# Performance work log

Measured on AMD Instinct MI355X. Metric: run time of the kernel, lower is better.

Reference implementation:

```python
import jax, jax.numpy as jnp
import numpy as np

# World configuration (2D layout ['h','w'])
B = 16            # batch
NH, NW = 64, 64   # token grid (token_sizes)
DO = 768          # dim_in + dim_coords
KH, KW = 16, 16   # kernel_sizes (patch extent, overlapping)
SH, SW = 8, 8     # patch_sizes (strides)
H, WF = 512, 512  # field_sizes
E = H * WF        # world.num_elements


def _build_fold_index():
    # idx[h, w, dh, dw] = clamp(h*SH+dh, 0, H-1)*WF + clamp(w*SW+dw, 0, WF-1)
    # mirrors FieldDecoder._build_fold_index with grid strides (WF, 1)
    ph = np.clip(np.arange(NH)[:, None] * SH + np.arange(KH)[None, :], 0, H - 1)   # [NH,KH]
    pw = np.clip(np.arange(NW)[:, None] * SW + np.arange(KW)[None, :], 0, WF - 1)  # [NW,KW]
    idx = ph[:, None, :, None] * WF + pw[None, :, None, :]                          # [NH,NW,KH,KW]
    return jnp.asarray(idx.reshape(-1), dtype=jnp.int32)


def setup_inputs() -> dict:
    key = jax.random.key(0)
    k1, k2 = jax.random.split(key)
    tgt = jax.random.normal(k1, (B, NH * NW, DO), dtype=jnp.float32)
    weight = jax.random.normal(k2, (KH, KW, DO), dtype=jnp.float32) * 0.02  # EinMix weight (k=v=1 absorbed)
    idx = _build_fold_index()
    return {"tgt": tgt, "weight": weight, "idx": idx}


def reference(tgt, weight, idx):
    # EinMix: 'b (h w) do -> b (h w hh ww)'  (shared per-patch projection, k=v=1)
    proj = jnp.einsum('bnd,xyd->bnxy', tgt, weight)          # [B, NH*NW, KH, KW]
    proj = proj.reshape(B, -1)                                # flat order (h, w, hh, ww) == idx layout
    # scatter_reduce(reduce='mean', include_self=False): sum then divide by counts
    sums = jnp.zeros((B, E), proj.dtype).at[:, idx].add(proj)
    counts = jnp.zeros((E,), proj.dtype).at[idx].add(1.0)     # every element is covered (kernel >= stride)
    field = sums / jnp.maximum(counts, 1.0)
    # unflatten_fields: 'b (flat) -> b h w'
    return field.reshape(B, H, WF)
```

## Files before the change

### kernel.cpp

```cpp
#include <hip/hip_runtime.h>
#include <hip/hip_bf16.h>

#define DIM      768
#define NPATCH   4096
#define BATCH    16
#define MROWS    (BATCH*NPATCH)
#define NCOLS    256
#define FH       512
#define FW       512

typedef __attribute__((ext_vector_type(8))) short bf16x8;
typedef __attribute__((ext_vector_type(4))) float f32x4;

static __device__ __forceinline__ unsigned short f2bf(float f) {
    union { float f; unsigned int u; } v; v.f = f;
    unsigned int u = v.u;
    return (unsigned short)((u + 0x7FFFu + ((u >> 16) & 1u)) >> 16);
}

__global__ void wconv_kernel(const float* __restrict__ w, unsigned short* __restrict__ wb) {
    int i = blockIdx.x * blockDim.x + threadIdx.x;
    float4 v = ((const float4*)w)[i];
    unsigned int p0 = (unsigned)f2bf(v.x) | ((unsigned)f2bf(v.y) << 16);
    unsigned int p1 = (unsigned)f2bf(v.z) | ((unsigned)f2bf(v.w) << 16);
    ((uint2*)wb)[i] = make_uint2(p0, p1);
}

#define BK 32
#define LSTR 40

__global__ __launch_bounds__(256) void gemm_kernel(const float* __restrict__ A,
                                                   const unsigned short* __restrict__ Bw,
                                                   float* __restrict__ C) {
    __shared__ unsigned short sA[128 * LSTR];
    __shared__ unsigned short sB[128 * LSTR];

    const int tid  = threadIdx.x;
    const int nblk = blockIdx.x;
    const int mblk = blockIdx.y;
    const int m0 = mblk * 128;
    const int n0 = nblk * 128;

    const int wave = tid >> 6;
    const int lane = tid & 63;
    const int wm = wave >> 1;
    const int wn = wave & 1;
    const int l15  = lane & 15;
    const int quad = lane >> 4;

    f32x4 acc[4][4] = {};

    const int arow = tid >> 3;
    const int ac4  = tid & 7;
    const int brow = tid >> 2;
    const int bc8  = tid & 3;

    for (int k0 = 0; k0 < DIM; k0 += BK) {
        __syncthreads();
        #pragma unroll
        for (int p = 0; p < 4; ++p) {
            int r = arow + p * 32;
            const float4 v = *(const float4*)(A + (size_t)(m0 + r) * DIM + k0 + ac4 * 4);
            unsigned int p0 = (unsigned)f2bf(v.x) | ((unsigned)f2bf(v.y) << 16);
            unsigned int p1 = (unsigned)f2bf(v.z) | ((unsigned)f2bf(v.w) << 16);
            *(uint2*)(&sA[r * LSTR + ac4 * 4]) = make_uint2(p0, p1);
        }
        #pragma unroll
        for (int p = 0; p < 2; ++p) {
            int r = brow + p * 64;
            const uint4 v = *(const uint4*)(Bw + (size_t)(n0 + r) * DIM + k0 + bc8 * 8);
            *(uint4*)(&sB[r * LSTR + bc8 * 8]) = v;
        }
        __syncthreads();

        bf16x8 af[4], bf[4];
        #pragma unroll
        for (int i = 0; i < 4; ++i)
            af[i] = *(const bf16x8*)(&sA[(wm * 64 + i * 16 + l15) * LSTR + quad * 8]);
        #pragma unroll
        for (int j = 0; j < 4; ++j)
            bf[j] = *(const bf16x8*)(&sB[(wn * 64 + j * 16 + l15) * LSTR + quad * 8]);
        #pragma unroll
        for (int i = 0; i < 4; ++i)
            #pragma unroll
            for (int j = 0; j < 4; ++j)
                acc[i][j] = __builtin_amdgcn_mfma_f32_16x16x32_bf16(af[i], bf[j], acc[i][j], 0, 0, 0);
    }

    #pragma unroll
    for (int i = 0; i < 4; ++i) {
        #pragma unroll
        for (int j = 0; j < 4; ++j) {
            const int col = n0 + wn * 64 + j * 16 + l15;
            #pragma unroll
            for (int r = 0; r < 4; ++r) {
                const int row = m0 + wm * 64 + i * 16 + quad * 4 + r;
                C[(size_t)row * NCOLS + col] = acc[i][j][r];
            }
        }
    }
}

__global__ void gather_kernel(const float* __restrict__ proj, float* __restrict__ out) {
    const int id = blockIdx.x * blockDim.x + threadIdx.x;
    const int b   = id >> 18;
    const int rem = id & 262143;
    const int ph  = rem >> 9;
    const int pw  = rem & 511;
    const float* p = proj + (size_t)b * (NPATCH * NCOLS);

    const int h_lo = (ph >= 8) ? ((ph - 8) >> 3) : 0;
    const int h_hi = ph >> 3;
    const int w_lo = (pw >= 8) ? ((pw - 8) >> 3) : 0;
    const int w_hi = pw >> 3;

    float sum = 0.f;
    for (int h = h_lo; h <= h_hi; ++h) {
        const int dh = ph - 8 * h;
        for (int w = w_lo; w <= w_hi; ++w) {
            const int dw = pw - 8 * w;
            sum += p[(h * 64 + w) * 256 + dh * 16 + dw];
        }
        if (pw == 511) {
            for (int dw = 8; dw < 16; ++dw)
                sum += p[(h * 64 + 63) * 256 + dh * 16 + dw];
        }
    }
    if (ph == 511) {
        for (int dh = 8; dh < 16; ++dh) {
            for (int w = w_lo; w <= w_hi; ++w) {
                const int dw = pw - 8 * w;
                sum += p[(63 * 64 + w) * 256 + dh * 16 + dw];
            }
            if (pw == 511) {
                for (int dw = 8; dw < 16; ++dw)
                    sum += p[(63 * 64 + 63) * 256 + dh * 16 + dw];
            }
        }
    }
    const int ch = (ph < 8) ? 1 : ((ph == 511) ? 10 : 2);
    const int cw = (pw < 8) ? 1 : ((pw == 511) ? 10 : 2);
    out[id] = sum / (float)(ch * cw);
}

extern "C" void kernel_launch(void* const* d_in, const int* in_sizes, int n_in,
                              void* d_out, int out_size, void* d_ws, size_t ws_size,
                              hipStream_t stream) {
    const float* tgt    = (const float*)d_in[0];
    const float* weight = (const float*)d_in[1];
    float* out = (float*)d_out;

    float* proj = (float*)d_ws;
    unsigned short* wbf =
        (unsigned short*)((char*)d_ws + (size_t)MROWS * NCOLS * sizeof(float));

    wconv_kernel<<<192, 256, 0, stream>>>(weight, wbf);

    dim3 grid(2, 512);
    gemm_kernel<<<grid, 256, 0, stream>>>(tgt, wbf, proj);

    gather_kernel<<<(BATCH * FH * FW) / 256, 256, 0, stream>>>(proj, out);
}
```

Measured before the change: 357.2 us.

## Store projection in bf16, prefetch GEMM tiles into registers, vectorize gather

The GEMM now writes its intermediate projection in bf16 instead of fp32, which halves the workspace write and the gather read traffic. The GEMM also loads the next K-tile into registers while the current one is computed, and uses a grouped 1D block mapping for L2 locality. The gather kernel now has each thread produce 8 contiguous output pixels with 16-byte loads and stores and multiplies by precomputed reciprocals instead of dividing. The cost is extra rounding error from the bf16 intermediate.

```diff
diff --git a/kernel.cpp b/kernel.cpp
--- a/kernel.cpp
+++ b/kernel.cpp
@@ -17,6 +17,9 @@
     unsigned int u = v.u;
     return (unsigned short)((u + 0x7FFFu + ((u >> 16) & 1u)) >> 16);
 }
+static __device__ __forceinline__ float bf2f(unsigned int u16) {
+    union { unsigned int i; float f; } x; x.i = u16 << 16; return x.f;
+}
 
 __global__ void wconv_kernel(const float* __restrict__ w, unsigned short* __restrict__ wb) {
     int i = blockIdx.x * blockDim.x + threadIdx.x;
@@ -31,13 +34,16 @@
 
 __global__ __launch_bounds__(256) void gemm_kernel(const float* __restrict__ A,
                                                    const unsigned short* __restrict__ Bw,
-                                                   float* __restrict__ C) {
+                                                   unsigned short* __restrict__ Cb) {
     __shared__ unsigned short sA[128 * LSTR];
     __shared__ unsigned short sB[128 * LSTR];
 
-    const int tid  = threadIdx.x;
-    const int nblk = blockIdx.x;
-    const int mblk = blockIdx.y;
+    const int tid = threadIdx.x;
+    const int lin  = blockIdx.x;
+    const int g    = lin >> 4;
+    const int r16  = lin & 15;
+    const int nblk = r16 >> 3;
+    const int mblk = g * 8 + (r16 & 7);
     const int m0 = mblk * 128;
     const int n0 = nblk * 128;
 
@@ -55,36 +61,52 @@
     const int brow = tid >> 2;
     const int bc8  = tid & 3;
 
+    const float*          aBase = A  + (size_t)(m0 + arow) * DIM + ac4 * 4;
+    const unsigned short* bBase = Bw + (size_t)(n0 + brow) * DIM + bc8 * 8;
+
+    float4 aReg[4];
+    uint4  bReg[2];
+    #pragma unroll
+    for (int p = 0; p < 4; ++p) aReg[p] = *(const float4*)(aBase + (size_t)p * 32 * DIM);
+    #pragma unroll
+    for (int p = 0; p < 2; ++p) bReg[p] = *(const uint4*)(bBase + (size_t)p * 64 * DIM);
+
+    #pragma unroll 1
     for (int k0 = 0; k0 < DIM; k0 += BK) {
         __syncthreads();
         #pragma unroll
         for (int p = 0; p < 4; ++p) {
-            int r = arow + p * 32;
-            const float4 v = *(const float4*)(A + (size_t)(m0 + r) * DIM + k0 + ac4 * 4);
+            const float4 v = aReg[p];
             unsigned int p0 = (unsigned)f2bf(v.x) | ((unsigned)f2bf(v.y) << 16);
             unsigned int p1 = (unsigned)f2bf(v.z) | ((unsigned)f2bf(v.w) << 16);
-            *(uint2*)(&sA[r * LSTR + ac4 * 4]) = make_uint2(p0, p1);
-        }
-        #pragma unroll
-        for (int p = 0; p < 2; ++p) {
-            int r = brow + p * 64;
-            const uint4 v = *(const uint4*)(Bw + (size_t)(n0 + r) * DIM + k0 + bc8 * 8);
-            *(uint4*)(&sB[r * LSTR + bc8 * 8]) = v;
-        }
+            *(uint2*)(&sA[(arow + p * 32) * LSTR + ac4 * 4]) = make_uint2(p0, p1);
+        }
+        #pragma unroll
+        for (int p = 0; p < 2; ++p)
+            *(uint4*)(&sB[(brow + p * 64) * LSTR + bc8 * 8]) = bReg[p];
         __syncthreads();
 
-        bf16x8 af[4], bf[4];
+        if (k0 + BK < DIM) {
+            #pragma unroll
+            for (int p = 0; p < 4; ++p)
+                aReg[p] = *(const float4*)(aBase + (size_t)p * 32 * DIM + k0 + BK);
+            #pragma unroll
+            for (int p = 0; p < 2; ++p)
+                bReg[p] = *(const uint4*)(bBase + (size_t)p * 64 * DIM + k0 + BK);
+        }
+
+        bf16x8 af[4], bfr[4];
         #pragma unroll
         for (int i = 0; i < 4; ++i)
             af[i] = *(const bf16x8*)(&sA[(wm * 64 + i * 16 + l15) * LSTR + quad * 8]);
         #pragma unroll
         for (int j = 0; j < 4; ++j)
-            bf[j] = *(const bf16x8*)(&sB[(wn * 64 + j * 16 + l15) * LSTR + quad * 8]);
+            bfr[j] = *(const bf16x8*)(&sB[(wn * 64 + j * 16 + l15) * LSTR + quad * 8]);
         #pragma unroll
         for (int i = 0; i < 4; ++i)
             #pragma unroll
             for (int j = 0; j < 4; ++j)
-                acc[i][j] = __builtin_amdgcn_mfma_f32_16x16x32_bf16(af[i], bf[j], acc[i][j], 0, 0, 0);
+                acc[i][j] = __builtin_amdgcn_mfma_f32_16x16x32_bf16(af[i], bfr[j], acc[i][j], 0, 0, 0);
     }
 
     #pragma unroll
@@ -93,54 +115,74 @@
         for (int j = 0; j < 4; ++j) {
             const int col = n0 + wn * 64 + j * 16 + l15;
             #pragma unroll
-            for (int r = 0; r < 4; ++r) {
-                const int row = m0 + wm * 64 + i * 16 + quad * 4 + r;
-                C[(size_t)row * NCOLS + col] = acc[i][j][r];
+            for (int rr = 0; rr < 4; ++rr) {
+                const int row = m0 + wm * 64 + i * 16 + quad * 4 + rr;
+                Cb[(size_t)row * NCOLS + col] = f2bf(acc[i][j][rr]);
             }
         }
     }
 }
 
-__global__ void gather_kernel(const float* __restrict__ proj, float* __restrict__ out) {
-    const int id = blockIdx.x * blockDim.x + threadIdx.x;
-    const int b   = id >> 18;
-    const int rem = id & 262143;
-    const int ph  = rem >> 9;
-    const int pw  = rem & 511;
-    const float* p = proj + (size_t)b * (NPATCH * NCOLS);
+__global__ void gather_kernel(const unsigned short* __restrict__ proj, float* __restrict__ out) {
+    const int id  = blockIdx.x * blockDim.x + threadIdx.x;
+    const int b   = id >> 15;
+    const int rem = id & 32767;
+    const int ph  = rem >> 6;
+    const int wg  = rem & 63;
+    const unsigned short* p = proj + (size_t)b * (NPATCH * NCOLS);
 
     const int h_lo = (ph >= 8) ? ((ph - 8) >> 3) : 0;
     const int h_hi = ph >> 3;
-    const int w_lo = (pw >= 8) ? ((pw - 8) >> 3) : 0;
-    const int w_hi = pw >> 3;
-
-    float sum = 0.f;
-    for (int h = h_lo; h <= h_hi; ++h) {
-        const int dh = ph - 8 * h;
-        for (int w = w_lo; w <= w_hi; ++w) {
-            const int dw = pw - 8 * w;
-            sum += p[(h * 64 + w) * 256 + dh * 16 + dw];
-        }
-        if (pw == 511) {
-            for (int dw = 8; dw < 16; ++dw)
-                sum += p[(h * 64 + 63) * 256 + dh * 16 + dw];
-        }
+
+    float s[8] = {0.f, 0.f, 0.f, 0.f, 0.f, 0.f, 0.f, 0.f};
+
+    auto contrib = [&](int h, int dh) {
+        const unsigned short* rowp = p + ((h * 64 + wg) * 256 + dh * 16);
+        const uint4 c0 = *(const uint4*)rowp;
+        const unsigned int w0[4] = {c0.x, c0.y, c0.z, c0.w};
+        #pragma unroll
+        for (int q = 0; q < 4; ++q) {
+            s[2 * q]     += bf2f(w0[q] & 0xFFFFu);
+            s[2 * q + 1] += bf2f(w0[q] >> 16);
+        }
+        if (wg > 0) {
+            const uint4 cm = *(const uint4*)(p + ((h * 64 + wg - 1) * 256 + dh * 16 + 8));
+            const unsigned int wm[4] = {cm.x, cm.y, cm.z, cm.w};
+            #pragma unroll
+            for (int q = 0; q < 4; ++q) {
+                s[2 * q]     += bf2f(wm[q] & 0xFFFFu);
+                s[2 * q + 1] += bf2f(wm[q] >> 16);
+            }
+        }
+        if (wg == 63) {
+            const uint4 ce = *(const uint4*)(rowp + 8);
+            const unsigned int we[4] = {ce.x, ce.y, ce.z, ce.w};
+            float e = 0.f;
+            #pragma unroll
+            for (int q = 0; q < 4; ++q)
+                e += bf2f(we[q] & 0xFFFFu) + bf2f(we[q] >> 16);
+            s[7] += e;
+        }
+    };
+
+    for (int h = h_lo; h <= h_hi; ++h) contrib(h, ph - 8 * h);
+    if (ph == 511) {
+        #pragma unroll 1
+        for (int dh = 8; dh < 16; ++dh) contrib(63, dh);
     }
-    if (ph == 511) {
-        for (int dh = 8; dh < 16; ++dh) {
-            for (int w = w_lo; w <= w_hi; ++w) {
-                const int dw = pw - 8 * w;
-                sum += p[(63 * 64 + w) * 256 + dh * 16 + dw];
-            }
-            if (pw == 511) {
-                for (int dw = 8; dw < 16; ++dw)
-                    sum += p[(63 * 64 + 63) * 256 + dh * 16 + dw];
-            }
-        }
-    }
-    const int ch = (ph < 8) ? 1 : ((ph == 511) ? 10 : 2);
-    const int cw = (pw < 8) ? 1 : ((pw == 511) ? 10 : 2);
-    out[id] = sum / (float)(ch * cw);
+
+    const float inv_ch = (ph < 8) ? 1.f : ((ph == 511) ? 0.1f : 0.5f);
+    const float inv_cw = (wg == 0) ? 1.f : 0.5f;
+    float f[8];
+    #pragma unroll
+    for (int j = 0; j < 8; ++j) f[j] = inv_ch * inv_cw;
+    if (wg == 63) f[7] = inv_ch * 0.1f;
+
+    float4 o0 = make_float4(s[0] * f[0], s[1] * f[1], s[2] * f[2], s[3] * f[3]);
+    float4 o1 = make_float4(s[4] * f[4], s[5] * f[5], s[6] * f[6], s[7] * f[7]);
+    float4* ob = (float4*)(out + (size_t)id * 8);
+    ob[0] = o0;
+    ob[1] = o1;
 }
 
 extern "C" void kernel_launch(void* const* d_in, const int* in_sizes, int n_in,
@@ -150,14 +192,10 @@
     const float* weight = (const float*)d_in[1];
     float* out = (float*)d_out;
 
-    float* proj = (float*)d_ws;
-    unsigned short* wbf =
-        (unsigned short*)((char*)d_ws + (size_t)MROWS * NCOLS * sizeof(float));
+    unsigned short* proj = (unsigned short*)d_ws;
+    unsigned short* wbf  = (unsigned short*)((char*)d_ws + (size_t)MROWS * NCOLS * 2);
 
     wconv_kernel<<<192, 256, 0, stream>>>(weight, wbf);
-
-    dim3 grid(2, 512);
-    gemm_kernel<<<grid, 256, 0, stream>>>(tgt, wbf, proj);
-
-    gather_kernel<<<(BATCH * FH * FW) / 256, 256, 0, stream>>>(proj, out);
-}
+    gemm_kernel<<<1024, 256, 0, stream>>>(tgt, wbf, proj);
+    gather_kernel<<<(BATCH * FH * 64) / 256, 256, 0, stream>>>(proj, out);
+}
```

New measurement: 379.3 us. 6.2% more time.

## Restructure GEMM to full-N tiles with bf16 output and LDS-tiled fold gather

Applied to the files above, without the earlier changes.

The GEMM now processes 64 rows by all 256 columns per block, so the fp32 activations are read and converted only once. It stages half the K range of A in LDS and streams B directly from global/L2. The projection is stored as bf16 through an LDS transpose for coalesced writes, which halves intermediate traffic. The gather kernel loads two patch rows into shared memory and writes float4 outputs using reciprocal multiplies instead of per-element global gathers and division. Rounding the intermediate to bf16 reduces precision.

```diff
diff --git a/kernel.cpp b/kernel.cpp
--- a/kernel.cpp
+++ b/kernel.cpp
@@ -4,18 +4,20 @@
 #define DIM      768
 #define NPATCH   4096
 #define BATCH    16
-#define MROWS    (BATCH*NPATCH)
+#define MROWS    65536
 #define NCOLS    256
-#define FH       512
-#define FW       512
 
 typedef __attribute__((ext_vector_type(8))) short bf16x8;
 typedef __attribute__((ext_vector_type(4))) float f32x4;
+typedef unsigned short ushort_t;
 
 static __device__ __forceinline__ unsigned short f2bf(float f) {
     union { float f; unsigned int u; } v; v.f = f;
     unsigned int u = v.u;
     return (unsigned short)((u + 0x7FFFu + ((u >> 16) & 1u)) >> 16);
+}
+static __device__ __forceinline__ float bf2f(unsigned int u16) {
+    union { unsigned int i; float f; } x; x.i = u16 << 16; return x.f;
 }
 
 __global__ void wconv_kernel(const float* __restrict__ w, unsigned short* __restrict__ wb) {
@@ -26,121 +28,148 @@
     ((uint2*)wb)[i] = make_uint2(p0, p1);
 }
 
-#define BK 32
-#define LSTR 40
+#define KHALF 384
+#define LSTRA 392
+#define CSTR  264
 
-__global__ __launch_bounds__(256) void gemm_kernel(const float* __restrict__ A,
-                                                   const unsigned short* __restrict__ Bw,
-                                                   float* __restrict__ C) {
-    __shared__ unsigned short sA[128 * LSTR];
-    __shared__ unsigned short sB[128 * LSTR];
+__global__ __launch_bounds__(256, 3) void gemm_kernel(const float* __restrict__ A,
+                                                      const unsigned short* __restrict__ Bw,
+                                                      unsigned short* __restrict__ Cb) {
+    __shared__ unsigned short sA[64 * LSTRA];
 
     const int tid  = threadIdx.x;
-    const int nblk = blockIdx.x;
-    const int mblk = blockIdx.y;
-    const int m0 = mblk * 128;
-    const int n0 = nblk * 128;
-
+    const int m0   = blockIdx.x * 64;
     const int wave = tid >> 6;
     const int lane = tid & 63;
-    const int wm = wave >> 1;
-    const int wn = wave & 1;
     const int l15  = lane & 15;
     const int quad = lane >> 4;
+    const int n0w  = wave * 64;
 
     f32x4 acc[4][4] = {};
 
-    const int arow = tid >> 3;
-    const int ac4  = tid & 7;
-    const int brow = tid >> 2;
-    const int bc8  = tid & 3;
+    const int srow = tid >> 2;
+    const int su   = tid & 3;
 
-    for (int k0 = 0; k0 < DIM; k0 += BK) {
+    const unsigned short* bBase[4];
+    #pragma unroll
+    for (int j = 0; j < 4; ++j)
+        bBase[j] = Bw + (size_t)(n0w + j * 16 + l15) * DIM + quad * 8;
+    const unsigned short* aBase = sA + l15 * LSTRA + quad * 8;
+
+    for (int half = 0; half < 2; ++half) {
+        const int kbase = half * KHALF;
         __syncthreads();
-        #pragma unroll
-        for (int p = 0; p < 4; ++p) {
-            int r = arow + p * 32;
-            const float4 v = *(const float4*)(A + (size_t)(m0 + r) * DIM + k0 + ac4 * 4);
-            unsigned int p0 = (unsigned)f2bf(v.x) | ((unsigned)f2bf(v.y) << 16);
-            unsigned int p1 = (unsigned)f2bf(v.z) | ((unsigned)f2bf(v.w) << 16);
-            *(uint2*)(&sA[r * LSTR + ac4 * 4]) = make_uint2(p0, p1);
-        }
-        #pragma unroll
-        for (int p = 0; p < 2; ++p) {
-            int r = brow + p * 64;
-            const uint4 v = *(const uint4*)(Bw + (size_t)(n0 + r) * DIM + k0 + bc8 * 8);
-            *(uint4*)(&sB[r * LSTR + bc8 * 8]) = v;
+        {
+            const float* aRow = A + (size_t)(m0 + srow) * DIM + kbase + su * 4;
+            unsigned short* dRow = sA + srow * LSTRA + su * 4;
+            #pragma unroll
+            for (int p = 0; p < 24; ++p) {
+                float4 v = *(const float4*)(aRow + p * 16);
+                unsigned int p0 = (unsigned)f2bf(v.x) | ((unsigned)f2bf(v.y) << 16);
+                unsigned int p1 = (unsigned)f2bf(v.z) | ((unsigned)f2bf(v.w) << 16);
+                *(uint2*)(dRow + p * 16) = make_uint2(p0, p1);
+            }
         }
         __syncthreads();
 
-        bf16x8 af[4], bf[4];
-        #pragma unroll
-        for (int i = 0; i < 4; ++i)
-            af[i] = *(const bf16x8*)(&sA[(wm * 64 + i * 16 + l15) * LSTR + quad * 8]);
+        #pragma unroll 4
+        for (int kk = 0; kk < 12; ++kk) {
+            bf16x8 bfr[4];
+            #pragma unroll
+            for (int j = 0; j < 4; ++j)
+                bfr[j] = *(const bf16x8*)(bBase[j] + kbase + kk * 32);
+            bf16x8 af[4];
+            #pragma unroll
+            for (int i = 0; i < 4; ++i)
+                af[i] = *(const bf16x8*)(aBase + i * 16 * LSTRA + kk * 32);
+            #pragma unroll
+            for (int i = 0; i < 4; ++i)
+                #pragma unroll
+                for (int j = 0; j < 4; ++j)
+                    acc[i][j] = __builtin_amdgcn_mfma_f32_16x16x32_bf16(af[i], bfr[j], acc[i][j], 0, 0, 0);
+        }
+    }
+
+    __syncthreads();
+    unsigned short* sC = sA;
+    #pragma unroll
+    for (int i = 0; i < 4; ++i)
         #pragma unroll
         for (int j = 0; j < 4; ++j)
-            bf[j] = *(const bf16x8*)(&sB[(wn * 64 + j * 16 + l15) * LSTR + quad * 8]);
-        #pragma unroll
-        for (int i = 0; i < 4; ++i)
             #pragma unroll
-            for (int j = 0; j < 4; ++j)
-                acc[i][j] = __builtin_amdgcn_mfma_f32_16x16x32_bf16(af[i], bf[j], acc[i][j], 0, 0, 0);
-    }
+            for (int rr = 0; rr < 4; ++rr)
+                sC[(i * 16 + quad * 4 + rr) * CSTR + n0w + j * 16 + l15] = f2bf(acc[i][j][rr]);
+    __syncthreads();
 
+    const int orow = tid >> 2;
+    const int ou   = tid & 3;
     #pragma unroll
-    for (int i = 0; i < 4; ++i) {
-        #pragma unroll
-        for (int j = 0; j < 4; ++j) {
-            const int col = n0 + wn * 64 + j * 16 + l15;
-            #pragma unroll
-            for (int r = 0; r < 4; ++r) {
-                const int row = m0 + wm * 64 + i * 16 + quad * 4 + r;
-                C[(size_t)row * NCOLS + col] = acc[i][j][r];
-            }
-        }
+    for (int p = 0; p < 8; ++p) {
+        uint4 v = *(const uint4*)(&sC[orow * CSTR + ou * 64 + p * 8]);
+        *(uint4*)(Cb + (size_t)(m0 + orow) * NCOLS + ou * 64 + p * 8) = v;
     }
 }
 
-__global__ void gather_kernel(const float* __restrict__ proj, float* __restrict__ out) {
-    const int id = blockIdx.x * blockDim.x + threadIdx.x;
-    const int b   = id >> 18;
-    const int rem = id & 262143;
-    const int ph  = rem >> 9;
-    const int pw  = rem & 511;
-    const float* p = proj + (size_t)b * (NPATCH * NCOLS);
+__global__ __launch_bounds__(256) void gather_kernel(const unsigned short* __restrict__ proj,
+                                                     float* __restrict__ out) {
+    __shared__ unsigned short sPrev[64 * 256];
+    __shared__ unsigned short sCur[64 * 256];
 
-    const int h_lo = (ph >= 8) ? ((ph - 8) >> 3) : 0;
-    const int h_hi = ph >> 3;
-    const int w_lo = (pw >= 8) ? ((pw - 8) >> 3) : 0;
-    const int w_hi = pw >> 3;
+    const int blk = blockIdx.x;
+    const int b   = blk >> 6;
+    const int h   = blk & 63;
+    const int tid = threadIdx.x;
+    const unsigned short* base = proj + (size_t)b * (NPATCH * NCOLS);
 
-    float sum = 0.f;
-    for (int h = h_lo; h <= h_hi; ++h) {
-        const int dh = ph - 8 * h;
-        for (int w = w_lo; w <= w_hi; ++w) {
-            const int dw = pw - 8 * w;
-            sum += p[(h * 64 + w) * 256 + dh * 16 + dw];
+    const uint4* gCur = (const uint4*)(base + (size_t)h * 64 * 256);
+    #pragma unroll
+    for (int p = 0; p < 8; ++p)
+        ((uint4*)sCur)[tid + p * 256] = gCur[tid + p * 256];
+    if (h > 0) {
+        const uint4* gPrev = (const uint4*)(base + (size_t)(h - 1) * 64 * 256);
+        #pragma unroll
+        for (int p = 0; p < 8; ++p)
+            ((uint4*)sPrev)[tid + p * 256] = gPrev[tid + p * 256];
+    }
+    __syncthreads();
+
+    const int r  = tid >> 5;
+    const int cg = tid & 31;
+    const int ph = h * 8 + r;
+
+    auto tapW = [&](const unsigned short* row, int dh, int pw) -> float {
+        const int w1 = pw >> 3, dw = pw & 7;
+        float v = bf2f(row[w1 * 256 + dh * 16 + dw]);
+        if (pw >= 8)
+            v += bf2f(row[(w1 - 1) * 256 + dh * 16 + dw + 8]);
+        if (pw == 511) {
+            #pragma unroll
+            for (int dwe = 8; dwe < 16; ++dwe)
+                v += bf2f(row[63 * 256 + dh * 16 + dwe]);
         }
-        if (pw == 511) {
-            for (int dw = 8; dw < 16; ++dw)
-                sum += p[(h * 64 + 63) * 256 + dh * 16 + dw];
+        return v;
+    };
+
+    const float inv_ch = (h == 0) ? 1.f : ((ph == 511) ? 0.1f : 0.5f);
+
+    float res[16];
+    #pragma unroll
+    for (int j = 0; j < 16; ++j) {
+        const int pw = cg * 16 + j;
+        float v = tapW(sCur, r, pw);
+        if (h > 0) v += tapW(sPrev, r + 8, pw);
+        if (ph == 511) {
+            #pragma unroll
+            for (int dh = 8; dh < 16; ++dh) v += tapW(sCur, dh, pw);
         }
+        const float inv_cw = (pw < 8) ? 1.f : ((pw == 511) ? 0.1f : 0.5f);
+        res[j] = v * inv_ch * inv_cw;
     }
-    if (ph == 511) {
-        for (int dh = 8; dh < 16; ++dh) {
-            for (int w = w_lo; w <= w_hi; ++w) {
-                const int dw = pw - 8 * w;
-                sum += p[(63 * 64 + w) * 256 + dh * 16 + dw];
-            }
-            if (pw == 511) {
-                for (int dw = 8; dw < 16; ++dw)
-                    sum += p[(63 * 64 + 63) * 256 + dh * 16 + dw];
-            }
-        }
-    }
-    const int ch = (ph < 8) ? 1 : ((ph == 511) ? 10 : 2);
-    const int cw = (pw < 8) ? 1 : ((pw == 511) ? 10 : 2);
-    out[id] = sum / (float)(ch * cw);
+
+    float* orow = out + ((size_t)(b * 512 + ph)) * 512 + cg * 16;
+    #pragma unroll
+    for (int q = 0; q < 4; ++q)
+        *(float4*)(orow + q * 4) = make_float4(res[4 * q], res[4 * q + 1], res[4 * q + 2], res[4 * q + 3]);
 }
 
 extern "C" void kernel_launch(void* const* d_in, const int* in_sizes, int n_in,
@@ -150,14 +179,10 @@
     const float* weight = (const float*)d_in[1];
     float* out = (float*)d_out;
 
-    float* proj = (float*)d_ws;
-    unsigned short* wbf =
-        (unsigned short*)((char*)d_ws + (size_t)MROWS * NCOLS * sizeof(float));
+    unsigned short* proj = (unsigned short*)d_ws;
+    unsigned short* wbf  = (unsigned short*)((char*)d_ws + (size_t)MROWS * NCOLS * 2);
 
     wconv_kernel<<<192, 256, 0, stream>>>(weight, wbf);
-
-    dim3 grid(2, 512);
-    gemm_kernel<<<grid, 256, 0, stream>>>(tgt, wbf, proj);
-
-    gather_kernel<<<(BATCH * FH * FW) / 256, 256, 0, stream>>>(proj, out);
+    gemm_kernel<<<MROWS / 64, 256, 0, stream>>>(tgt, wbf, proj);
+    gather_kernel<<<BATCH * 64, 256, 0, stream>>>(proj, out);
 }
```

Result: slower. 371.9 us (+4.1%).
